# Performance work log

Hardware: AMD Instinct MI355X
Metric: run time of the kernel (lower is better)

Reference implementation:

```python
import math
import jax, jax.numpy as jnp
import numpy as np

H = 12  # n_heads
NEG = -1e9

def setup_inputs() -> dict:
    key = jax.random.key(0)
    ks = jax.random.split(key, 5)
    B, S, D = 1, 4096, 768
    x = jax.random.normal(ks[0], (B, S, D), dtype=jnp.float32)
    Wqkv = jax.random.normal(ks[1], (D, 3 * D), dtype=jnp.float32) * (1.0 / math.sqrt(D))
    bqkv = jnp.zeros((3 * D,), dtype=jnp.float32)
    Wout = jax.random.normal(ks[2], (D, D), dtype=jnp.float32) * (1.0 / math.sqrt(D))
    bout = jnp.zeros((D,), dtype=jnp.float32)
    rel_bias = jax.random.normal(ks[3], (H, S, S), dtype=jnp.float32) * 0.02
    # additive causal mask: 0 on/below diagonal, large negative above
    causal_mask = jnp.where(jnp.tril(jnp.ones((S, S), dtype=bool)), 0.0, NEG).astype(jnp.float32)
    return {"x": x, "Wqkv": Wqkv, "bqkv": bqkv, "Wout": Wout, "bout": bout,
            "rel_bias": rel_bias, "causal_mask": causal_mask}

def reference(x, Wqkv, bqkv, Wout, bout, rel_bias, causal_mask):
    B, S, D = x.shape
    hd = D // H
    qkv = x @ Wqkv + bqkv                      # [B,S,3D]
    q, k, v = jnp.split(qkv, 3, axis=-1)
    def heads(t):  # [B,S,D] -> [B,H,S,hd]
        return t.reshape(B, S, H, hd).transpose(0, 2, 1, 3)
    q, k, v = heads(q), heads(k), heads(v)
    scores = jnp.einsum('bhqd,bhkd->bhqk', q, k) / math.sqrt(hd)
    scores = scores + rel_bias[None] + causal_mask[None, None]
    attn = jax.nn.softmax(scores, axis=-1)     # dropout p=0.0 -> identity
    out = jnp.einsum('bhqk,bhkd->bhqd', attn, v)
    out = out.transpose(0, 2, 1, 3).reshape(B, S, D)
    return out @ Wout + bout
```

## Files before the change

kernel.cpp:

```cpp
#include <hip/hip_runtime.h>
#include <stdint.h>

typedef _Float16 f16;
typedef _Float16 f16x8 __attribute__((ext_vector_type(8)));
typedef _Float16 f16x4 __attribute__((ext_vector_type(4)));
typedef float f32x4 __attribute__((ext_vector_type(4)));

#define NEGF -1e30f

static __device__ __forceinline__ f32x4 mfma16(f16x8 a, f16x8 b, f32x4 c) {
    return __builtin_amdgcn_mfma_f32_16x16x32_f16(a, b, c, 0, 0, 0);
}

static __device__ __forceinline__ void gload_lds16(const void* g, void* l) {
    __builtin_amdgcn_global_load_lds(
        (const __attribute__((address_space(1))) unsigned int*)g,
        (__attribute__((address_space(3))) unsigned int*)l, 16, 0, 0);
}

__global__ void cast_f32_f16(const float* __restrict__ src, f16* __restrict__ dst, int n) {
    int idx = blockIdx.x * blockDim.x + threadIdx.x;
    int stride = gridDim.x * blockDim.x;
    for (int i = idx * 4; i < n; i += stride * 4) {
        float4 v = *(const float4*)(src + i);
        f16x4 h;
        h[0] = (f16)v.x; h[1] = (f16)v.y; h[2] = (f16)v.z; h[3] = (f16)v.w;
        *(f16x4*)(dst + i) = h;
    }
}

__global__ void transpose_cast(const float* __restrict__ src, f16* __restrict__ dst, int R, int C) {
    __shared__ float tile[32][33];
    const int c0 = blockIdx.x * 32, r0 = blockIdx.y * 32;
    const int tx = threadIdx.x & 31, ty = threadIdx.x >> 5;
#pragma unroll
    for (int i = 0; i < 32; i += 8)
        tile[ty + i][tx] = src[(size_t)(r0 + ty + i) * C + c0 + tx];
    __syncthreads();
#pragma unroll
    for (int i = 0; i < 32; i += 8)
        dst[(size_t)(c0 + ty + i) * R + r0 + tx] = (f16)tile[tx][ty + i];
}

__global__ void __launch_bounds__(256, 2)
gemm_qkv(const f16* __restrict__ A, const f16* __restrict__ Bt,
         const float* __restrict__ bias,
         f16* __restrict__ Qb, f16* __restrict__ Kb, f16* __restrict__ Vtb, int K) {
    __shared__ alignas(16) f16 As[2][128 * 32];
    __shared__ alignas(16) f16 Bs[2][128 * 32];
    const int t = threadIdx.x;
    const int lane = t & 63, wid = t >> 6;
    const int wm = wid >> 1, wn = wid & 1;
    const int lr = lane & 15, lg = lane >> 4;
    const int m0 = blockIdx.y * 128, n0 = blockIdx.x * 128;

    auto stage = [&](int buf, int k0) {
#pragma unroll
        for (int i = 0; i < 2; i++) {
            const int cc = t + i * 256;
            const int rr = cc >> 2, ch = cc & 3;
            gload_lds16(A + (size_t)(m0 + rr) * K + k0 + ch * 8, (f16*)As[buf] + cc * 8);
            gload_lds16(Bt + (size_t)(n0 + rr) * K + k0 + ch * 8, (f16*)Bs[buf] + cc * 8);
        }
    };

    f32x4 acc[4][4] = {};
    stage(0, 0);
    __syncthreads();
    const int NK = K / 32;
    for (int it = 0; it < NK; ++it) {
        const int cur = it & 1;
        if (it + 1 < NK) stage(cur ^ 1, (it + 1) * 32);
        f16x8 af[4], bf[4];
#pragma unroll
        for (int i = 0; i < 4; i++)
            af[i] = *(const f16x8*)((f16*)As[cur] + (wm * 64 + i * 16 + lr) * 32 + lg * 8);
#pragma unroll
        for (int j = 0; j < 4; j++)
            bf[j] = *(const f16x8*)((f16*)Bs[cur] + (wn * 64 + j * 16 + lr) * 32 + lg * 8);
#pragma unroll
        for (int i = 0; i < 4; i++)
#pragma unroll
            for (int j = 0; j < 4; j++)
                acc[i][j] = mfma16(af[i], bf[j], acc[i][j]);
        __syncthreads();
    }
#pragma unroll
    for (int i = 0; i < 4; i++) {
#pragma unroll
        for (int j = 0; j < 4; j++) {
            const int n_g = n0 + wn * 64 + j * 16 + lr;
            const float bv = bias[n_g];
#pragma unroll
            for (int jj = 0; jj < 4; jj++) {
                const int m_g = m0 + wm * 64 + i * 16 + lg * 4 + jj;
                const float val = acc[i][j][jj] + bv;
                if (n_g < 768) {
                    Qb[(((n_g >> 6) * 4096) + m_g) * 64 + (n_g & 63)] = (f16)(val * 0.125f);
                } else if (n_g < 1536) {
                    const int n2 = n_g - 768;
                    Kb[(((n2 >> 6) * 4096) + m_g) * 64 + (n2 & 63)] = (f16)val;
                } else {
                    const int n2 = n_g - 1536;
                    Vtb[((n2 >> 6) * 64 + (n2 & 63)) * 4096 + m_g] = (f16)val;
                }
            }
        }
    }
}

__global__ void __launch_bounds__(256, 3)
gemm_out(const f16* __restrict__ A, const f16* __restrict__ Bt,
         const float* __restrict__ bias, float* __restrict__ Cout, int K, int N) {
    __shared__ alignas(16) f16 As[2][128 * 32];
    __shared__ alignas(16) f16 Bs[2][64 * 32];
    const int t = threadIdx.x;
    const int lane = t & 63, wid = t >> 6;
    const int lr = lane & 15, lg = lane >> 4;
    const int m0 = blockIdx.y * 128, n0 = blockIdx.x * 64;

    auto stage = [&](int buf, int k0) {
#pragma unroll
        for (int i = 0; i < 2; i++) {
            const int cc = t + i * 256;
            const int rr = cc >> 2, ch = cc & 3;
            gload_lds16(A + (size_t)(m0 + rr) * K + k0 + ch * 8, (f16*)As[buf] + cc * 8);
        }
        const int rr = t >> 2, ch = t & 3;
        gload_lds16(Bt + (size_t)(n0 + rr) * K + k0 + ch * 8, (f16*)Bs[buf] + t * 8);
    };

    f32x4 acc[2][4] = {};
    stage(0, 0);
    __syncthreads();
    const int NK = K / 32;
    for (int it = 0; it < NK; ++it) {
        const int cur = it & 1;
        if (it + 1 < NK) stage(cur ^ 1, (it + 1) * 32);
        f16x8 af[2], bf[4];
#pragma unroll
        for (int i = 0; i < 2; i++)
            af[i] = *(const f16x8*)((f16*)As[cur] + (wid * 32 + i * 16 + lr) * 32 + lg * 8);
#pragma unroll
        for (int j = 0; j < 4; j++)
            bf[j] = *(const f16x8*)((f16*)Bs[cur] + (j * 16 + lr) * 32 + lg * 8);
#pragma unroll
        for (int i = 0; i < 2; i++)
#pragma unroll
            for (int j = 0; j < 4; j++)
                acc[i][j] = mfma16(af[i], bf[j], acc[i][j]);
        __syncthreads();
    }
#pragma unroll
    for (int i = 0; i < 2; i++) {
#pragma unroll
        for (int j = 0; j < 4; j++) {
            const int n_g = n0 + j * 16 + lr;
            const float bv = bias[n_g];
#pragma unroll
            for (int jj = 0; jj < 4; jj++) {
                const int m_g = m0 + wid * 32 + i * 16 + lg * 4 + jj;
                Cout[(size_t)m_g * N + n_g] = acc[i][j][jj] + bv;
            }
        }
    }
}

__global__ void __launch_bounds__(256, 3)
attn_fwd(const f16* __restrict__ Qb, const f16* __restrict__ Kb,
         const f16* __restrict__ Vtb, const float* __restrict__ rel_bias,
         f16* __restrict__ Opart, float* __restrict__ mpart, float* __restrict__ lpart) {
    __shared__ alignas(16) f16 Ks[2][64 * 64];
    __shared__ alignas(16) f16 Vs[2][64 * 64];
    __shared__ alignas(16) f16 Ps[4][32 * 72];
    __shared__ alignas(16) float fac[4][32];
    const int bid = blockIdx.x;
    const int h = bid / 144;
    int rr = bid % 144;
    int qb = 0;
    for (;;) { const int n = (qb + 4) >> 2; if (rr < n) break; rr -= n; ++qb; }
    const int c = rr;
    const int lo = c * 8;
    const int hi = min(lo + 8, 2 * qb + 2);

    const int t = threadIdx.x, lane = t & 63, wid = t >> 6;
    const int lr = lane & 15, lg = lane >> 4;
    const int g = qb * 4 + wid;
    const int q0w = g * 32;
    const int ktd = g >> 1;
    const f16* Qh = Qb + (size_t)h * 4096 * 64;
    const f16* Kh = Kb + (size_t)h * 4096 * 64;
    const f16* Vh = Vtb + (size_t)h * 64 * 4096;
    const float* rbh = rel_bias + (size_t)h * 4096 * 4096;

    auto stage = [&](int buf, int kt) {
        const int kbase = kt * 64;
#pragma unroll
        for (int i = 0; i < 2; i++) {
            const int cc = t + i * 256;
            const int row = cc >> 3;
            const int cswz = (((cc & 7) * 16) ^ ((row & 7) << 4)) >> 1;
            gload_lds16(Kh + (size_t)(kbase + row) * 64 + cswz, (f16*)Ks[buf] + cc * 8);
            gload_lds16(Vh + (size_t)row * 4096 + kbase + cswz, (f16*)Vs[buf] + cc * 8);
        }
    };

    f16x8 qf[2][2];
#pragma unroll
    for (int nf = 0; nf < 2; nf++)
#pragma unroll
        for (int kd = 0; kd < 2; kd++)
            qf[nf][kd] = *(const f16x8*)(Qh + (size_t)(q0w + nf * 16 + lr) * 64 + kd * 32 + lg * 8);

    f32x4 o[2][4] = {};
    float mrow[2] = {NEGF, NEGF};
    float lrow[2] = {0.f, 0.f};

    stage(0, lo);
    __syncthreads();
    for (int kt = lo; kt < hi; kt++) {
        const int kbase = kt * 64;
        const int cur = (kt - lo) & 1;
        if (kt + 1 < hi) stage(cur ^ 1, kt + 1);
        if (kt <= ktd) {
            float4 rb[2][4];
#pragma unroll
            for (int nf = 0; nf < 2; nf++)
#pragma unroll
                for (int mf = 0; mf < 4; mf++)
                    rb[nf][mf] = *(const float4*)(rbh + (size_t)(q0w + nf * 16 + lr) * 4096 + kbase + mf * 16 + lg * 4);
            f32x4 st[4][2] = {};
#pragma unroll
            for (int kd = 0; kd < 2; kd++) {
#pragma unroll
                for (int mf = 0; mf < 4; mf++) {
                    const int r = mf * 16 + lr;
                    const int cf = ((kd * 64 + lg * 16) ^ ((r & 7) << 4)) >> 1;
                    const f16x8 kf = *(const f16x8*)((f16*)Ks[cur] + r * 64 + cf);
#pragma unroll
                    for (int nf = 0; nf < 2; nf++)
                        st[mf][nf] = mfma16(kf, qf[nf][kd], st[mf][nf]);
                }
            }
            const bool diag = (kt == ktd);
#pragma unroll
            for (int nf = 0; nf < 2; nf++) {
                const int q_g = q0w + nf * 16 + lr;
                float mx = NEGF;
#pragma unroll
                for (int mf = 0; mf < 4; mf++) {
                    const float rbv[4] = {rb[nf][mf].x, rb[nf][mf].y, rb[nf][mf].z, rb[nf][mf].w};
#pragma unroll
                    for (int jj = 0; jj < 4; jj++) {
                        float v = st[mf][nf][jj] + rbv[jj];
                        if (diag) {
                            const int k_g = kbase + mf * 16 + lg * 4 + jj;
                            v = (k_g > q_g) ? NEGF : v;
                        }
                        st[mf][nf][jj] = v;
                        mx = fmaxf(mx, v);
                    }
                }
                mx = fmaxf(mx, __shfl_xor(mx, 16));
                mx = fmaxf(mx, __shfl_xor(mx, 32));
                const float mnew = fmaxf(mrow[nf], mx);
                const float fscale = __expf(mrow[nf] - mnew);
                mrow[nf] = mnew;
                float rsum = 0.f;
#pragma unroll
                for (int mf = 0; mf < 4; mf++) {
                    f16x4 pv;
#pragma unroll
                    for (int jj = 0; jj < 4; jj++) {
                        const float p = __expf(st[mf][nf][jj] - mnew);
                        rsum += p;
                        pv[jj] = (f16)p;
                    }
                    *(f16x4*)(&Ps[wid][(nf * 16 + lr) * 72 + mf * 16 + lg * 4]) = pv;
                }
                rsum += __shfl_xor(rsum, 16);
                rsum += __shfl_xor(rsum, 32);
                lrow[nf] = lrow[nf] * fscale + rsum;
                if (lane < 16) fac[wid][nf * 16 + lr] = fscale;
            }
            asm volatile("s_waitcnt lgkmcnt(0)" ::: "memory");
#pragma unroll
            for (int qf2 = 0; qf2 < 2; qf2++) {
                const float4 fv = *(const float4*)&fac[wid][qf2 * 16 + lg * 4];
                const float fvv[4] = {fv.x, fv.y, fv.z, fv.w};
#pragma unroll
                for (int df = 0; df < 4; df++)
#pragma unroll
                    for (int jj = 0; jj < 4; jj++)
                        o[qf2][df][jj] *= fvv[jj];
            }
#pragma unroll
            for (int kk = 0; kk < 2; kk++) {
                f16x8 pa[2], vb[4];
#pragma unroll
                for (int qf2 = 0; qf2 < 2; qf2++)
                    pa[qf2] = *(const f16x8*)(&Ps[wid][(qf2 * 16 + lr) * 72 + kk * 32 + lg * 8]);
#pragma unroll
                for (int df = 0; df < 4; df++) {
                    const int r = df * 16 + lr;
                    const int cf = ((kk * 64 + lg * 16) ^ ((r & 7) << 4)) >> 1;
                    vb[df] = *(const f16x8*)((f16*)Vs[cur] + r * 64 + cf);
                }
#pragma unroll
                for (int qf2 = 0; qf2 < 2; qf2++)
#pragma unroll
                    for (int df = 0; df < 4; df++)
                        o[qf2][df] = mfma16(pa[qf2], vb[df], o[qf2][df]);
            }
        }
        __syncthreads();
    }

    const int s = (h * 128 + g) * 8 + c;
    f16* Op = Opart + (size_t)s * 2048;
#pragma unroll
    for (int qf2 = 0; qf2 < 2; qf2++)
#pragma unroll
        for (int df = 0; df < 4; df++)
#pragma unroll
            for (int jj = 0; jj < 4; jj++)
                Op[(qf2 * 16 + lg * 4 + jj) * 64 + df * 16 + lr] = (f16)o[qf2][df][jj];
    if (lg == 0) {
#pragma unroll
        for (int nf = 0; nf < 2; nf++) {
            mpart[(size_t)s * 32 + nf * 16 + lr] = mrow[nf];
            lpart[(size_t)s * 32 + nf * 16 + lr] = lrow[nf];
        }
    }
}

__global__ void __launch_bounds__(256)
merge_norm(const f16* __restrict__ Opart, const float* __restrict__ mpart,
           const float* __restrict__ lpart, f16* __restrict__ Ob) {
    __shared__ float wls[8][32];
    __shared__ float Linv[32];
    const int g = blockIdx.x, h = blockIdx.y;
    const int nc = (g >> 4) + 1;
    const size_t sb = (size_t)(h * 128 + g) * 8;
    const int t = threadIdx.x;
    if (t < 32) {
        float M = NEGF;
#pragma unroll
        for (int i = 0; i < 8; i++)
            if (i < nc) M = fmaxf(M, mpart[(sb + i) * 32 + t]);
        float L = 0.f;
#pragma unroll
        for (int i = 0; i < 8; i++)
            if (i < nc) {
                const float w = __expf(mpart[(sb + i) * 32 + t] - M);
                wls[i][t] = w;
                L += w * lpart[(sb + i) * 32 + t];
            }
        Linv[t] = 1.f / L;
    }
    __syncthreads();
    const int row = t >> 3, dq = t & 7;
    float acc[8] = {};
#pragma unroll
    for (int i = 0; i < 8; i++) {
        if (i < nc) {
            const f16x8 a = *(const f16x8*)(Opart + (sb + i) * 2048 + row * 64 + dq * 8);
            const float w = wls[i][row];
#pragma unroll
            for (int j = 0; j < 8; j++) acc[j] += w * (float)a[j];
        }
    }
    const float inv = Linv[row];
    const int q = g * 32 + row;
    f16x8 ov;
#pragma unroll
    for (int j = 0; j < 8; j++) ov[j] = (f16)(acc[j] * inv);
    *(f16x8*)(Ob + (size_t)q * 768 + h * 64 + dq * 8) = ov;
}

extern "C" void kernel_launch(void* const* d_in, const int* in_sizes, int n_in,
                              void* d_out, int out_size, void* d_ws, size_t ws_size,
                              hipStream_t stream) {
    const float* x = (const float*)d_in[0];
    const float* Wqkv = (const float*)d_in[1];
    const float* bqkv = (const float*)d_in[2];
    const float* Wout = (const float*)d_in[3];
    const float* bout = (const float*)d_in[4];
    const float* rel_bias = (const float*)d_in[5];
    float* out = (float*)d_out;

    f16* p = (f16*)d_ws;
    f16* xb = p;     p += (size_t)4096 * 768;
    f16* WqkvT = p;  p += (size_t)2304 * 768;
    f16* WoutT = p;  p += (size_t)768 * 768;
    f16* Qb = p;     p += (size_t)12 * 4096 * 64;
    f16* Kb = p;     p += (size_t)12 * 4096 * 64;
    f16* Vtb = p;    p += (size_t)12 * 4096 * 64;
    f16* Ob = p;     p += (size_t)4096 * 768;
    f16* Opart = p;  p += (size_t)12 * 128 * 8 * 2048;
    float* fp = (float*)p;
    float* mpart = fp;  fp += (size_t)12 * 128 * 8 * 32;
    float* lpart = fp;  fp += (size_t)12 * 128 * 8 * 32;

    cast_f32_f16<<<3072, 256, 0, stream>>>(x, xb, 4096 * 768);
    transpose_cast<<<dim3(2304 / 32, 768 / 32), 256, 0, stream>>>(Wqkv, WqkvT, 768, 2304);
    transpose_cast<<<dim3(768 / 32, 768 / 32), 256, 0, stream>>>(Wout, WoutT, 768, 768);
    gemm_qkv<<<dim3(18, 32), 256, 0, stream>>>(xb, WqkvT, bqkv, Qb, Kb, Vtb, 768);
    attn_fwd<<<dim3(1728), 256, 0, stream>>>(Qb, Kb, Vtb, rel_bias, Opart, mpart, lpart);
    merge_norm<<<dim3(128, 12), 256, 0, stream>>>(Opart, mpart, lpart, Ob);
    gemm_out<<<dim3(12, 32), 256, 0, stream>>>(Ob, WoutT, bout, out, 768, 768);
}
```

Before: 199.4 us.

## Prefetch next tile's relative bias, use exp2 softmax, shuffle rescale factors

Moves the rel_bias load for the next key tile so it is issued one iteration ahead, overlapping the dominant fp32 bias stream with compute, and replaces __syncthreads with a manual vmcnt wait plus s_barrier so the pending bias loads are not drained at each barrier. The softmax switches from __expf to exp2f with a pre-multiplied log2(e) via fma. The LDS round-trip for the per-row rescale factors is replaced by cross-lane shuffles. The hand-counted vmcnt(8) relies on an exact count of outstanding loads and could break correctness if the compiler reorders or splits them; prefetched registers also raise register pressure under the 3-block launch bound.

```diff
diff --git a/kernel.cpp b/kernel.cpp
--- a/kernel.cpp
+++ b/kernel.cpp
@@ -173,7 +173,6 @@
     __shared__ alignas(16) f16 Ks[2][64 * 64];
     __shared__ alignas(16) f16 Vs[2][64 * 64];
     __shared__ alignas(16) f16 Ps[4][32 * 72];
-    __shared__ alignas(16) float fac[4][32];
     const int bid = blockIdx.x;
     const int h = bid / 144;
     int rr = bid % 144;
@@ -215,20 +214,32 @@
     f32x4 o[2][4] = {};
     float mrow[2] = {NEGF, NEGF};
     float lrow[2] = {0.f, 0.f};
+    float4 rb[2][4];
+    auto biasPrefetch = [&](int kt) {
+#pragma unroll
+        for (int nf = 0; nf < 2; nf++)
+#pragma unroll
+            for (int mf = 0; mf < 4; mf++)
+                rb[nf][mf] = *(const float4*)(rbh + (size_t)(q0w + nf * 16 + lr) * 4096 + kt * 64 + mf * 16 + lg * 4);
+    };
+    const float L2E = 1.4426950408889634f;
 
     stage(0, lo);
-    __syncthreads();
+    if (lo <= ktd) {
+        biasPrefetch(lo);
+        asm volatile("s_waitcnt vmcnt(8)" ::: "memory");
+    } else {
+        asm volatile("s_waitcnt vmcnt(0)" ::: "memory");
+    }
+    __builtin_amdgcn_s_barrier();
+    asm volatile("" ::: "memory");
+
     for (int kt = lo; kt < hi; kt++) {
         const int kbase = kt * 64;
         const int cur = (kt - lo) & 1;
         if (kt + 1 < hi) stage(cur ^ 1, kt + 1);
+        const bool nextBias = (kt + 1 <= ktd) && (kt + 1 < hi);
         if (kt <= ktd) {
-            float4 rb[2][4];
-#pragma unroll
-            for (int nf = 0; nf < 2; nf++)
-#pragma unroll
-                for (int mf = 0; mf < 4; mf++)
-                    rb[nf][mf] = *(const float4*)(rbh + (size_t)(q0w + nf * 16 + lr) * 4096 + kbase + mf * 16 + lg * 4);
             f32x4 st[4][2] = {};
 #pragma unroll
             for (int kd = 0; kd < 2; kd++) {
@@ -243,6 +254,7 @@
                 }
             }
             const bool diag = (kt == ktd);
+            float fs2[2];
 #pragma unroll
             for (int nf = 0; nf < 2; nf++) {
                 const int q_g = q0w + nf * 16 + lr;
@@ -264,7 +276,8 @@
                 mx = fmaxf(mx, __shfl_xor(mx, 16));
                 mx = fmaxf(mx, __shfl_xor(mx, 32));
                 const float mnew = fmaxf(mrow[nf], mx);
-                const float fscale = __expf(mrow[nf] - mnew);
+                const float m2 = mnew * L2E;
+                fs2[nf] = exp2f(mrow[nf] * L2E - m2);
                 mrow[nf] = mnew;
                 float rsum = 0.f;
 #pragma unroll
@@ -272,7 +285,7 @@
                     f16x4 pv;
 #pragma unroll
                     for (int jj = 0; jj < 4; jj++) {
-                        const float p = __expf(st[mf][nf][jj] - mnew);
+                        const float p = exp2f(__builtin_fmaf(st[mf][nf][jj], L2E, -m2));
                         rsum += p;
                         pv[jj] = (f16)p;
                     }
@@ -280,19 +293,18 @@
                 }
                 rsum += __shfl_xor(rsum, 16);
                 rsum += __shfl_xor(rsum, 32);
-                lrow[nf] = lrow[nf] * fscale + rsum;
-                if (lane < 16) fac[wid][nf * 16 + lr] = fscale;
-            }
-            asm volatile("s_waitcnt lgkmcnt(0)" ::: "memory");
+                lrow[nf] = lrow[nf] * fs2[nf] + rsum;
+            }
+            if (nextBias) biasPrefetch(kt + 1);
 #pragma unroll
             for (int qf2 = 0; qf2 < 2; qf2++) {
-                const float4 fv = *(const float4*)&fac[wid][qf2 * 16 + lg * 4];
-                const float fvv[4] = {fv.x, fv.y, fv.z, fv.w};
-#pragma unroll
-                for (int df = 0; df < 4; df++)
-#pragma unroll
-                    for (int jj = 0; jj < 4; jj++)
-                        o[qf2][df][jj] *= fvv[jj];
+#pragma unroll
+                for (int jj = 0; jj < 4; jj++) {
+                    const float f = __shfl(fs2[qf2], lg * 4 + jj);
+#pragma unroll
+                    for (int df = 0; df < 4; df++)
+                        o[qf2][df][jj] *= f;
+                }
             }
 #pragma unroll
             for (int kk = 0; kk < 2; kk++) {
@@ -313,7 +325,10 @@
                         o[qf2][df] = mfma16(pa[qf2], vb[df], o[qf2][df]);
             }
         }
-        __syncthreads();
+        if (nextBias) asm volatile("s_waitcnt vmcnt(8)" ::: "memory");
+        else          asm volatile("s_waitcnt vmcnt(0)" ::: "memory");
+        __builtin_amdgcn_s_barrier();
+        asm volatile("" ::: "memory");
     }
 
     const int s = (h * 128 + g) * 8 + c;
```

Result: slower. 236.2 us (+18.5%).
